# Kernel tuning notes

Hardware: AMD Instinct MI355X
Metric: run time of the kernel (lower is better)

The kernel has to match this reference:

```python
import jax, jax.numpy as jnp
import numpy as np
import math

BLOCK_SIZE = 512

def _block_attention(query, key, value):
    # query/key/value: [B, S, H, D]; block-wise attention with PER-BLOCK softmax
    # and normalizer accumulation, faithful to _ring_attention_single (causal, no dropout).
    B, S, H, D = query.shape
    bs = BLOCK_SIZE
    nb = S // bs
    scale = 1.0 / math.sqrt(D)
    neg = jnp.where(jnp.triu(jnp.ones((bs, bs), dtype=bool), 1), -jnp.inf, 0.0)  # strict-upper causal mask for diagonal block
    outs = []
    for i in range(nb):  # small fixed number of blocks (8)
        qb = query[:, i * bs:(i + 1) * bs]                      # [B, bs, H, D]
        kb = key[:, :(i + 1) * bs]                              # [B, (i+1)*bs, H, D]
        vb = value[:, :(i + 1) * bs].reshape(B, i + 1, bs, H, D)
        s = jnp.einsum('bqhd,bkhd->bhqk', qb, kb) * scale       # [B, H, bs, (i+1)*bs]
        s = s.reshape(B, H, bs, i + 1, bs)
        s = s.at[:, :, :, i, :].add(neg)                        # causal mask on diagonal block j == i
        p = jax.nn.softmax(s, axis=-1)                          # softmax PER kv block (faithful to source)
        o = jnp.einsum('bhqjk,bjkhd->bqhd', p, vb)              # accumulated block outputs
        norm = p.sum(axis=-1).sum(axis=-1)                      # [B, H, bs] accumulated normalizer (== i+1 per row)
        norm = jnp.clip(norm, 1e-6, None).transpose(0, 2, 1)[..., None]  # [B, bs, H, 1]
        outs.append(o / norm)
    return jnp.concatenate(outs, axis=1)  # [B, S, H, D]


def setup_inputs() -> dict:
    key = jax.random.key(0)
    k1, k2, k3 = jax.random.split(key, 3)
    shape = (2, 4096, 16, 128)
    return {
        'query': jax.random.normal(k1, shape, dtype=jnp.float32),
        'key': jax.random.normal(k2, shape, dtype=jnp.float32),
        'value': jax.random.normal(k3, shape, dtype=jnp.float32),
    }


def reference(query, key, value):
    return _block_attention(query, key, value)
```

## Files before the change

kernel.cpp:

```cpp
#include <hip/hip_runtime.h>

typedef short bf16x8 __attribute__((ext_vector_type(8)));
typedef short bf16x4 __attribute__((ext_vector_type(4)));
typedef float f32x4  __attribute__((ext_vector_type(4)));
typedef unsigned int u32;
typedef u32 u32x2 __attribute__((ext_vector_type(2)));

#define SEQ 4096
#define NH  16
#define HD  128

__device__ __forceinline__ short bf16_rne(float x) {
  u32 u = __builtin_bit_cast(u32, x);
  u = (u + 0x7FFFu + ((u >> 16) & 1u)) >> 16;
  return (short)u;
}

typedef __attribute__((address_space(1))) const void as1c_void;
typedef __attribute__((address_space(3))) void as3_void;

__global__ __launch_bounds__(256) void prep_k(const float* __restrict__ K,
                                              short* __restrict__ Kp) {
  int idx = blockIdx.x * 256 + threadIdx.x;
  int d4 = idx & 31;
  int s  = (idx >> 5) & 4095;
  int h  = (idx >> 17) & 15;
  int b  = idx >> 21;
  f32x4 v = *(const f32x4*)(K + (((size_t)(b * SEQ + s) * NH + h) << 7) + d4 * 4);
  bf16x4 o;
  o[0] = bf16_rne(v[0]); o[1] = bf16_rne(v[1]);
  o[2] = bf16_rne(v[2]); o[3] = bf16_rne(v[3]);
  int x = (d4 * 4) ^ ((s & 7) << 3);
  *(bf16x4*)(Kp + (((size_t)(b * NH + h) * SEQ + s) << 7) + x) = o;
}

__global__ __launch_bounds__(256) void prep_v(const float* __restrict__ V,
                                              short* __restrict__ Vt) {
  __shared__ short tile[64 * 128];
  int bid = blockIdx.x;
  int sb = bid & 63;
  int h  = (bid >> 6) & 15;
  int b  = bid >> 10;
  int t = threadIdx.x;
  {
    int s = t >> 2;
    int dbase = (t & 3) * 32;
    const float* src = V + (((size_t)(b * SEQ + sb * 64 + s) * NH + h) << 7) + dbase;
    int sw = (s & 7) << 3;
#pragma unroll
    for (int j = 0; j < 8; ++j) {
      f32x4 v = *(const f32x4*)(src + j * 4);
      bf16x4 o;
      o[0] = bf16_rne(v[0]); o[1] = bf16_rne(v[1]);
      o[2] = bf16_rne(v[2]); o[3] = bf16_rne(v[3]);
      int d = dbase + j * 4;
      *(bf16x4*)&tile[s * 128 + (d ^ sw)] = o;
    }
  }
  __syncthreads();
  {
    int w = t >> 6, l = t & 63, g = l >> 4, lq = l & 15;
    int srel = lq * 4;
#pragma unroll
    for (int j = 0; j < 8; ++j) {
      int d = w * 32 + j * 4 + g;
      bf16x4 o;
#pragma unroll
      for (int i = 0; i < 4; ++i) {
        int s = srel + i;
        o[i] = tile[s * 128 + (d ^ ((s & 7) << 3))];
      }
      int sp = srel ^ ((d & 7) << 3);
      *(bf16x4*)(Vt + (((size_t)(b * NH + h) * HD + d) << 12) + sb * 64 + sp) = o;
    }
  }
}

__global__ __launch_bounds__(512, 4) void attn_main(const float* __restrict__ Q,
                                                    const short* __restrict__ Kp,
                                                    const short* __restrict__ Vt,
                                                    float* __restrict__ Out) {
  __shared__ __align__(16) short sK[2][64 * 128];
  __shared__ __align__(16) short sV[2][128 * 64];
  __shared__ __align__(16) short sP[8][16 * 64];

  int bid0 = (int)blockIdx.x;
  int bid = (bid0 & 7) * 64 + (bid0 >> 3);
  int p  = bid & 15;
  int h  = (bid >> 4) & 15;
  int b  = bid >> 8;

  int tid = threadIdx.x;
  int l = tid & 63, w = tid >> 6;
  int g = l >> 4, lq = l & 15;
  int rxor = (lq & 7) << 3;
  int cx[4];
#pragma unroll
  for (int i = 0; i < 4; ++i) cx[i] = (i * 32 + g * 8) ^ rxor;

  const short* Kb = Kp + ((size_t)(b * NH + h) << 19);
  const short* Vb = Vt + ((size_t)(b * NH + h) << 19);

  const char* kga0 = (const char*)Kb + w * 2048 + l * 16;
  const char* vga0_0 = (const char*)Vb + (size_t)(w * 16 + (l >> 3)) * 8192 + (l & 7) * 16;
  const char* vga1_0 = vga0_0 + 8 * 8192;

  const float SCL = 0.08838834764831845f * 1.4426950408889634f;

  for (int ts = 0; ts < 2; ++ts) {
    int qt = ts ? p : (31 - p);
    int iblk = qt >> 2;
    int qrow0 = qt * 128 + w * 16;
    int qg = qrow0 + lq;
    int qrel = (qt & 3) * 128 + w * 16;
    int nch_w = (qt & 3) * 2 + (w >> 2) + 1;
    int ntot = 8 * iblk + (qt & 3) * 2 + 2;

    bf16x8 qf[4];
    {
      const float* qp = Q + (((size_t)(b * SEQ + qg) * NH + h) << 7);
#pragma unroll
      for (int i = 0; i < 4; ++i) {
        int d0 = i * 32 + g * 8;
        f32x4 a = *(const f32x4*)(qp + d0);
        f32x4 c2 = *(const f32x4*)(qp + d0 + 4);
        bf16x8 f;
        f[0] = bf16_rne(a[0] * SCL);  f[1] = bf16_rne(a[1] * SCL);
        f[2] = bf16_rne(a[2] * SCL);  f[3] = bf16_rne(a[3] * SCL);
        f[4] = bf16_rne(c2[0] * SCL); f[5] = bf16_rne(c2[1] * SCL);
        f[6] = bf16_rne(c2[2] * SCL); f[7] = bf16_rne(c2[3] * SCL);
        qf[i] = f;
      }
    }

    f32x4 ot[8];
#pragma unroll
    for (int i = 0; i < 8; ++i) ot[i] = (f32x4){0.f, 0.f, 0.f, 0.f};
    f32x4 ob[8];
#pragma unroll
    for (int i = 0; i < 8; ++i) ob[i] = (f32x4){0.f, 0.f, 0.f, 0.f};
    float Z = 0.0f;

    const char* kg = kga0;
    const char* vg0 = vga0_0;
    const char* vg1 = vga1_0;

    __syncthreads();
    {
      char* kl = (char*)&sK[0][0] + w * 2048;
      char* vl = (char*)&sV[0][0] + w * 2048;
      __builtin_amdgcn_global_load_lds((as1c_void*)kg, (as3_void*)kl, 16, 0, 0);
      __builtin_amdgcn_global_load_lds((as1c_void*)(kg + 1024), (as3_void*)(kl + 1024), 16, 0, 0);
      __builtin_amdgcn_global_load_lds((as1c_void*)vg0, (as3_void*)vl, 16, 0, 0);
      __builtin_amdgcn_global_load_lds((as1c_void*)vg1, (as3_void*)(vl + 1024), 16, 0, 0);
    }

#pragma unroll 2
    for (int t = 0; t < ntot; ++t) {
      __syncthreads();

      if (t + 1 < ntot) {
        kg += 16384; vg0 += 128; vg1 += 128;
        char* kl = (char*)&sK[(t + 1) & 1][0] + w * 2048;
        char* vl = (char*)&sV[(t + 1) & 1][0] + w * 2048;
        __builtin_amdgcn_global_load_lds((as1c_void*)kg, (as3_void*)kl, 16, 0, 0);
        __builtin_amdgcn_global_load_lds((as1c_void*)(kg + 1024), (as3_void*)(kl + 1024), 16, 0, 0);
        __builtin_amdgcn_global_load_lds((as1c_void*)vg0, (as3_void*)vl, 16, 0, 0);
        __builtin_amdgcn_global_load_lds((as1c_void*)vg1, (as3_void*)(vl + 1024), 16, 0, 0);
      }

      int jb = t >> 3, c = t & 7;
      const int diag = (jb == iblk);

      if (!(diag && c >= nch_w)) {
        const short* kb = sK[t & 1];
        const short* vb = sV[t & 1];

        f32x4 st[4];
        __builtin_amdgcn_s_setprio(1);
#pragma unroll
        for (int t4 = 0; t4 < 4; ++t4) {
          f32x4 acc = (f32x4){0.f, 0.f, 0.f, 0.f};
          int rb = (t4 * 16 + lq) << 7;
#pragma unroll
          for (int i = 0; i < 4; ++i) {
            bf16x8 kf = *(const bf16x8*)&kb[rb + cx[i]];
            acc = __builtin_amdgcn_mfma_f32_16x16x32_bf16(kf, qf[i], acc, 0, 0, 0);
          }
          st[t4] = acc;
        }
        __builtin_amdgcn_s_setprio(0);

        if (diag && (c * 64 + 63 > qrel)) {
          int kb0 = jb * 512 + c * 64;
#pragma unroll
          for (int t4 = 0; t4 < 4; ++t4) {
#pragma unroll
            for (int r = 0; r < 4; ++r) {
              if (kb0 + t4 * 16 + g * 4 + r > qg) st[t4][r] = -1e30f;
            }
          }
        }

        float csum = 0.0f;
#pragma unroll
        for (int t4 = 0; t4 < 4; ++t4) {
          float p0 = __builtin_amdgcn_exp2f(st[t4][0]);
          float p1 = __builtin_amdgcn_exp2f(st[t4][1]);
          float p2 = __builtin_amdgcn_exp2f(st[t4][2]);
          float p3 = __builtin_amdgcn_exp2f(st[t4][3]);
          csum += (p0 + p1) + (p2 + p3);
          u32x2 pk;
          asm("v_cvt_pk_bf16_f32 %0, %1, %2" : "=v"(pk[0]) : "v"(p0), "v"(p1));
          asm("v_cvt_pk_bf16_f32 %0, %1, %2" : "=v"(pk[1]) : "v"(p2), "v"(p3));
          *(u32x2*)&sP[w][(lq << 6) + ((t4 * 16 + g * 4) ^ rxor)] = pk;
        }
        Z += csum;

        __builtin_amdgcn_s_setprio(1);
#pragma unroll
        for (int ksx = 0; ksx < 2; ++ksx) {
          bf16x8 pa = *(const bf16x8*)&sP[w][(lq << 6) + cx[ksx]];
#pragma unroll
          for (int dt = 0; dt < 8; ++dt) {
            bf16x8 vbf = *(const bf16x8*)&vb[((dt * 16 + lq) << 6) + cx[ksx]];
            ob[dt] = __builtin_amdgcn_mfma_f32_16x16x32_bf16(pa, vbf, ob[dt], 0, 0, 0);
          }
        }
        __builtin_amdgcn_s_setprio(0);
      }

      if ((t & 7) == 7 || t == ntot - 1) {
        float zf = Z;
        zf += __shfl_xor(zf, 16, 64);
        zf += __shfl_xor(zf, 32, 64);
#pragma unroll
        for (int r = 0; r < 4; ++r) {
          float Zr = __shfl(zf, (l & 48) | (g * 4 + r), 64);
          float rz = 1.0f / Zr;
#pragma unroll
          for (int dt = 0; dt < 8; ++dt) ot[dt][r] += ob[dt][r] * rz;
        }
#pragma unroll
        for (int i = 0; i < 8; ++i) ob[i] = (f32x4){0.f, 0.f, 0.f, 0.f};
        Z = 0.0f;
      }
    }

    float rnorm = 1.0f / (float)(iblk + 1);
#pragma unroll
    for (int dt = 0; dt < 8; ++dt) {
#pragma unroll
      for (int r = 0; r < 4; ++r) {
        int qrow = qrow0 + g * 4 + r;
        Out[(((size_t)(b * SEQ + qrow) * NH + h) << 7) + dt * 16 + lq] = ot[dt][r] * rnorm;
      }
    }
  }
}

extern "C" void kernel_launch(void* const* d_in, const int* in_sizes, int n_in,
                              void* d_out, int out_size, void* d_ws, size_t ws_size,
                              hipStream_t stream) {
  const float* Q = (const float*)d_in[0];
  const float* K = (const float*)d_in[1];
  const float* V = (const float*)d_in[2];
  float* out = (float*)d_out;

  short* Kp = (short*)d_ws;
  short* Vt = Kp + (size_t)2 * NH * SEQ * HD;

  prep_k<<<(2 * NH * SEQ * (HD / 4)) / 256, 256, 0, stream>>>(K, Kp);
  prep_v<<<2 * NH * (SEQ / 64), 256, 0, stream>>>(V, Vt);
  attn_main<<<2 * NH * 16, 512, 0, stream>>>(Q, Kp, Vt, out);
}
```

Baseline: 217.8 us.

## Switch attention to 32x32x16 MFMA with register-resident P via permlane swap

The main attention kernel now uses 4 waves of 32 query rows each with 32x32x16 bf16 MFMAs instead of 8 waves of 16 rows with 16x16x32. The softmax probabilities are repacked in registers with v_permlane32_swap, so the LDS round-trip through sP and its buffer are gone. Block size drops to 256 threads and each thread issues more async global-to-LDS loads. This aims to raise MFMA efficiency and cut LDS traffic, at the cost of higher register pressure, fewer waves per block and possible occupancy loss.

```diff
diff --git a/kernel.cpp b/kernel.cpp
--- a/kernel.cpp
+++ b/kernel.cpp
@@ -3,8 +3,9 @@
 typedef short bf16x8 __attribute__((ext_vector_type(8)));
 typedef short bf16x4 __attribute__((ext_vector_type(4)));
 typedef float f32x4  __attribute__((ext_vector_type(4)));
+typedef float f32x16 __attribute__((ext_vector_type(16)));
 typedef unsigned int u32;
-typedef u32 u32x2 __attribute__((ext_vector_type(2)));
+typedef u32 u32x4 __attribute__((ext_vector_type(4)));
 
 #define SEQ 4096
 #define NH  16
@@ -18,6 +19,9 @@
 
 typedef __attribute__((address_space(1))) const void as1c_void;
 typedef __attribute__((address_space(3))) void as3_void;
+
+#define CVTPK(d, a, b) asm("v_cvt_pk_bf16_f32 %0, %1, %2" : "=v"(d) : "v"(a), "v"(b))
+#define PLSWAP(x, y)   asm("v_permlane32_swap_b32 %0, %1" : "+v"(x), "+v"(y))
 
 __global__ __launch_bounds__(256) void prep_k(const float* __restrict__ K,
                                               short* __restrict__ Kp) {
@@ -76,13 +80,12 @@
   }
 }
 
-__global__ __launch_bounds__(512, 4) void attn_main(const float* __restrict__ Q,
+__global__ __launch_bounds__(256, 2) void attn_main(const float* __restrict__ Q,
                                                     const short* __restrict__ Kp,
                                                     const short* __restrict__ Vt,
                                                     float* __restrict__ Out) {
   __shared__ __align__(16) short sK[2][64 * 128];
   __shared__ __align__(16) short sV[2][128 * 64];
-  __shared__ __align__(16) short sP[8][16 * 64];
 
   int bid0 = (int)blockIdx.x;
   int bid = (bid0 & 7) * 64 + (bid0 >> 3);
@@ -92,36 +95,48 @@
 
   int tid = threadIdx.x;
   int l = tid & 63, w = tid >> 6;
-  int g = l >> 4, lq = l & 15;
-  int rxor = (lq & 7) << 3;
-  int cx[4];
-#pragma unroll
-  for (int i = 0; i < 4; ++i) cx[i] = (i * 32 + g * 8) ^ rxor;
-
-  const short* Kb = Kp + ((size_t)(b * NH + h) << 19);
-  const short* Vb = Vt + ((size_t)(b * NH + h) << 19);
-
-  const char* kga0 = (const char*)Kb + w * 2048 + l * 16;
-  const char* vga0_0 = (const char*)Vb + (size_t)(w * 16 + (l >> 3)) * 8192 + (l & 7) * 16;
-  const char* vga1_0 = vga0_0 + 8 * 8192;
+  int q5 = l & 31;
+  int hi = l >> 5;
+  int hi4 = hi * 4, hi8 = hi * 8;
+  int cswz = (l & 7) << 4;
+
+  int kcol[8], vcol[4];
+#pragma unroll
+  for (int i = 0; i < 8; ++i) kcol[i] = (i * 32 + hi * 16) ^ cswz;
+#pragma unroll
+  for (int ks = 0; ks < 4; ++ks) vcol[ks] = (ks * 32 + hi * 16) ^ cswz;
+
+  const int pat[16] = {0,1,2,3, 8,9,10,11, 16,17,18,19, 24,25,26,27};
+
+  const char* KbB = (const char*)(Kp + ((size_t)(b * NH + h) << 19));
+  const char* VbB = (const char*)(Vt + ((size_t)(b * NH + h) << 19));
+
+  const char* kgb[4]; const char* vgb[4]; int ldo[4];
+#pragma unroll
+  for (int j = 0; j < 4; ++j) {
+    int idx = j * 256 + tid;
+    kgb[j] = KbB + idx * 16;
+    vgb[j] = VbB + (size_t)(idx >> 3) * 8192 + (idx & 7) * 16;
+    ldo[j] = idx * 16;
+  }
 
   const float SCL = 0.08838834764831845f * 1.4426950408889634f;
 
   for (int ts = 0; ts < 2; ++ts) {
     int qt = ts ? p : (31 - p);
     int iblk = qt >> 2;
-    int qrow0 = qt * 128 + w * 16;
-    int qg = qrow0 + lq;
-    int qrel = (qt & 3) * 128 + w * 16;
-    int nch_w = (qt & 3) * 2 + (w >> 2) + 1;
+    int qrow0 = qt * 128 + w * 32;
+    int qg = qrow0 + q5;
+    int qgrel = (qt & 3) * 128 + w * 32 + q5;
+    int nch_w = (qt & 3) * 2 + (w >> 1) + 1;
     int ntot = 8 * iblk + (qt & 3) * 2 + 2;
 
-    bf16x8 qf[4];
+    bf16x8 qf[8];
     {
       const float* qp = Q + (((size_t)(b * SEQ + qg) * NH + h) << 7);
 #pragma unroll
-      for (int i = 0; i < 4; ++i) {
-        int d0 = i * 32 + g * 8;
+      for (int i = 0; i < 8; ++i) {
+        int d0 = i * 16 + hi8;
         f32x4 a = *(const f32x4*)(qp + d0);
         f32x4 c2 = *(const f32x4*)(qp + d0 + 4);
         bf16x8 f;
@@ -133,26 +148,19 @@
       }
     }
 
-    f32x4 ot[8];
-#pragma unroll
-    for (int i = 0; i < 8; ++i) ot[i] = (f32x4){0.f, 0.f, 0.f, 0.f};
-    f32x4 ob[8];
-#pragma unroll
-    for (int i = 0; i < 8; ++i) ob[i] = (f32x4){0.f, 0.f, 0.f, 0.f};
+    f32x16 ot[4], ob[4];
+#pragma unroll
+    for (int dt = 0; dt < 4; ++dt) {
+#pragma unroll
+      for (int r = 0; r < 16; ++r) { ot[dt][r] = 0.f; ob[dt][r] = 0.f; }
+    }
     float Z = 0.0f;
 
-    const char* kg = kga0;
-    const char* vg0 = vga0_0;
-    const char* vg1 = vga1_0;
-
     __syncthreads();
-    {
-      char* kl = (char*)&sK[0][0] + w * 2048;
-      char* vl = (char*)&sV[0][0] + w * 2048;
-      __builtin_amdgcn_global_load_lds((as1c_void*)kg, (as3_void*)kl, 16, 0, 0);
-      __builtin_amdgcn_global_load_lds((as1c_void*)(kg + 1024), (as3_void*)(kl + 1024), 16, 0, 0);
-      __builtin_amdgcn_global_load_lds((as1c_void*)vg0, (as3_void*)vl, 16, 0, 0);
-      __builtin_amdgcn_global_load_lds((as1c_void*)vg1, (as3_void*)(vl + 1024), 16, 0, 0);
+#pragma unroll
+    for (int j = 0; j < 4; ++j) {
+      __builtin_amdgcn_global_load_lds((as1c_void*)kgb[j], (as3_void*)((char*)sK[0] + ldo[j]), 16, 0, 0);
+      __builtin_amdgcn_global_load_lds((as1c_void*)vgb[j], (as3_void*)((char*)sV[0] + ldo[j]), 16, 0, 0);
     }
 
 #pragma unroll 2
@@ -160,100 +168,102 @@
       __syncthreads();
 
       if (t + 1 < ntot) {
-        kg += 16384; vg0 += 128; vg1 += 128;
-        char* kl = (char*)&sK[(t + 1) & 1][0] + w * 2048;
-        char* vl = (char*)&sV[(t + 1) & 1][0] + w * 2048;
-        __builtin_amdgcn_global_load_lds((as1c_void*)kg, (as3_void*)kl, 16, 0, 0);
-        __builtin_amdgcn_global_load_lds((as1c_void*)(kg + 1024), (as3_void*)(kl + 1024), 16, 0, 0);
-        __builtin_amdgcn_global_load_lds((as1c_void*)vg0, (as3_void*)vl, 16, 0, 0);
-        __builtin_amdgcn_global_load_lds((as1c_void*)vg1, (as3_void*)(vl + 1024), 16, 0, 0);
+        int bi = (t + 1) & 1;
+#pragma unroll
+        for (int j = 0; j < 4; ++j) {
+          __builtin_amdgcn_global_load_lds((as1c_void*)(kgb[j] + (size_t)(t + 1) * 16384),
+                                           (as3_void*)((char*)sK[bi] + ldo[j]), 16, 0, 0);
+          __builtin_amdgcn_global_load_lds((as1c_void*)(vgb[j] + (size_t)(t + 1) * 128),
+                                           (as3_void*)((char*)sV[bi] + ldo[j]), 16, 0, 0);
+        }
       }
 
       int jb = t >> 3, c = t & 7;
       const int diag = (jb == iblk);
 
       if (!(diag && c >= nch_w)) {
-        const short* kb = sK[t & 1];
-        const short* vb = sV[t & 1];
-
-        f32x4 st[4];
+        const char* kbuf = (const char*)sK[t & 1];
+        const char* vbuf = (const char*)sV[t & 1];
+        bf16x8 pa[4];
+        float csum = 0.0f;
+
+#pragma unroll
+        for (int kt = 0; kt < 2; ++kt) {
+          f32x16 st;
+#pragma unroll
+          for (int r = 0; r < 16; ++r) st[r] = 0.f;
+          int rowb = kt * 8192 + q5 * 256;
+          __builtin_amdgcn_s_setprio(1);
+#pragma unroll
+          for (int i = 0; i < 8; ++i) {
+            bf16x8 kf = *(const bf16x8*)(kbuf + rowb + kcol[i]);
+            st = __builtin_amdgcn_mfma_f32_32x32x16_bf16(kf, qf[i], st, 0, 0, 0);
+          }
+          __builtin_amdgcn_s_setprio(0);
+
+          if (diag && c == nch_w - 1) {
+            int lim = qgrel - (c * 64 + kt * 32);
+#pragma unroll
+            for (int r = 0; r < 16; ++r) {
+              if (pat[r] + hi4 > lim) st[r] = -1e30f;
+            }
+          }
+
+          float pr[16];
+#pragma unroll
+          for (int r = 0; r < 16; ++r) {
+            pr[r] = __builtin_amdgcn_exp2f(st[r]);
+            csum += pr[r];
+          }
+          u32 X0, X1, Y0, Y1;
+          CVTPK(X0, pr[0], pr[1]); CVTPK(X1, pr[2], pr[3]);
+          CVTPK(Y0, pr[4], pr[5]); CVTPK(Y1, pr[6], pr[7]);
+          PLSWAP(X0, Y0); PLSWAP(X1, Y1);
+          pa[kt * 2] = __builtin_bit_cast(bf16x8, (u32x4){X0, X1, Y0, Y1});
+          u32 A0, A1, B0, B1;
+          CVTPK(A0, pr[8], pr[9]);   CVTPK(A1, pr[10], pr[11]);
+          CVTPK(B0, pr[12], pr[13]); CVTPK(B1, pr[14], pr[15]);
+          PLSWAP(A0, B0); PLSWAP(A1, B1);
+          pa[kt * 2 + 1] = __builtin_bit_cast(bf16x8, (u32x4){A0, A1, B0, B1});
+        }
+        Z += csum;
+
         __builtin_amdgcn_s_setprio(1);
 #pragma unroll
-        for (int t4 = 0; t4 < 4; ++t4) {
-          f32x4 acc = (f32x4){0.f, 0.f, 0.f, 0.f};
-          int rb = (t4 * 16 + lq) << 7;
-#pragma unroll
-          for (int i = 0; i < 4; ++i) {
-            bf16x8 kf = *(const bf16x8*)&kb[rb + cx[i]];
-            acc = __builtin_amdgcn_mfma_f32_16x16x32_bf16(kf, qf[i], acc, 0, 0, 0);
-          }
-          st[t4] = acc;
+        for (int ks = 0; ks < 4; ++ks) {
+#pragma unroll
+          for (int dt = 0; dt < 4; ++dt) {
+            bf16x8 vf = *(const bf16x8*)(vbuf + (dt * 32 + q5) * 128 + vcol[ks]);
+            ob[dt] = __builtin_amdgcn_mfma_f32_32x32x16_bf16(pa[ks], vf, ob[dt], 0, 0, 0);
+          }
         }
         __builtin_amdgcn_s_setprio(0);
-
-        if (diag && (c * 64 + 63 > qrel)) {
-          int kb0 = jb * 512 + c * 64;
-#pragma unroll
-          for (int t4 = 0; t4 < 4; ++t4) {
-#pragma unroll
-            for (int r = 0; r < 4; ++r) {
-              if (kb0 + t4 * 16 + g * 4 + r > qg) st[t4][r] = -1e30f;
-            }
-          }
-        }
-
-        float csum = 0.0f;
-#pragma unroll
-        for (int t4 = 0; t4 < 4; ++t4) {
-          float p0 = __builtin_amdgcn_exp2f(st[t4][0]);
-          float p1 = __builtin_amdgcn_exp2f(st[t4][1]);
-          float p2 = __builtin_amdgcn_exp2f(st[t4][2]);
-          float p3 = __builtin_amdgcn_exp2f(st[t4][3]);
-          csum += (p0 + p1) + (p2 + p3);
-          u32x2 pk;
-          asm("v_cvt_pk_bf16_f32 %0, %1, %2" : "=v"(pk[0]) : "v"(p0), "v"(p1));
-          asm("v_cvt_pk_bf16_f32 %0, %1, %2" : "=v"(pk[1]) : "v"(p2), "v"(p3));
-          *(u32x2*)&sP[w][(lq << 6) + ((t4 * 16 + g * 4) ^ rxor)] = pk;
-        }
-        Z += csum;
-
-        __builtin_amdgcn_s_setprio(1);
-#pragma unroll
-        for (int ksx = 0; ksx < 2; ++ksx) {
-          bf16x8 pa = *(const bf16x8*)&sP[w][(lq << 6) + cx[ksx]];
-#pragma unroll
-          for (int dt = 0; dt < 8; ++dt) {
-            bf16x8 vbf = *(const bf16x8*)&vb[((dt * 16 + lq) << 6) + cx[ksx]];
-            ob[dt] = __builtin_amdgcn_mfma_f32_16x16x32_bf16(pa, vbf, ob[dt], 0, 0, 0);
-          }
-        }
-        __builtin_amdgcn_s_setprio(0);
       }
 
       if ((t & 7) == 7 || t == ntot - 1) {
-        float zf = Z;
-        zf += __shfl_xor(zf, 16, 64);
-        zf += __shfl_xor(zf, 32, 64);
-#pragma unroll
-        for (int r = 0; r < 4; ++r) {
-          float Zr = __shfl(zf, (l & 48) | (g * 4 + r), 64);
-          float rz = 1.0f / Zr;
-#pragma unroll
-          for (int dt = 0; dt < 8; ++dt) ot[dt][r] += ob[dt][r] * rz;
-        }
-#pragma unroll
-        for (int i = 0; i < 8; ++i) ob[i] = (f32x4){0.f, 0.f, 0.f, 0.f};
+        float zf = Z + __shfl_xor(Z, 32, 64);
+        float rz[16];
+#pragma unroll
+        for (int r = 0; r < 16; ++r) rz[r] = 1.0f / __shfl(zf, pat[r] + hi4, 64);
+#pragma unroll
+        for (int dt = 0; dt < 4; ++dt) {
+#pragma unroll
+          for (int r = 0; r < 16; ++r) {
+            ot[dt][r] += ob[dt][r] * rz[r];
+            ob[dt][r] = 0.f;
+          }
+        }
         Z = 0.0f;
       }
     }
 
     float rnorm = 1.0f / (float)(iblk + 1);
 #pragma unroll
-    for (int dt = 0; dt < 8; ++dt) {
-#pragma unroll
-      for (int r = 0; r < 4; ++r) {
-        int qrow = qrow0 + g * 4 + r;
-        Out[(((size_t)(b * SEQ + qrow) * NH + h) << 7) + dt * 16 + lq] = ot[dt][r] * rnorm;
+    for (int dt = 0; dt < 4; ++dt) {
+#pragma unroll
+      for (int r = 0; r < 16; ++r) {
+        int qrow = qrow0 + pat[r] + hi4;
+        Out[(((size_t)(b * SEQ + qrow) * NH + h) << 7) + dt * 32 + q5] = ot[dt][r] * rnorm;
       }
     }
   }
@@ -272,5 +282,5 @@
 
   prep_k<<<(2 * NH * SEQ * (HD / 4)) / 256, 256, 0, stream>>>(K, Kp);
   prep_v<<<2 * NH * (SEQ / 64), 256, 0, stream>>>(V, Vt);
-  attn_main<<<2 * NH * 16, 512, 0, stream>>>(Q, Kp, Vt, out);
-}
+  attn_main<<<2 * NH * 16, 256, 0, stream>>>(Q, Kp, Vt, out);
+}
```

New measurement: 212.1 us. 1.03x faster.
